# Performance work log

Measured on AMD Instinct MI355X. Metric: run time of the kernel, lower is better.

## Reference

```python
import jax, jax.numpy as jnp
import numpy as np

N_NODES = 200000
N_EDGES = 6400000
NUM_FEATURES = 128


def _glorot(key, fan_in, fan_out):
    return jax.random.normal(key, (fan_in, fan_out), jnp.float32) * (1.0 / np.sqrt(fan_in))


def gcn_conv(x, src, dst, W, b):
    """PyG GCNConv: h = D^{-1/2}(A+I)D^{-1/2} (x @ W) + b, self-loops added."""
    n = x.shape[0]
    ones = jnp.ones(src.shape, x.dtype)
    # degree after adding self-loops: 1 + in-degree (edges flow src -> dst)
    deg = 1.0 + jax.ops.segment_sum(ones, dst, num_segments=n)
    dinv = jax.lax.rsqrt(deg)  # deg >= 1, safe
    h = x @ W  # [n, out]
    norm = dinv[src] * dinv[dst]  # [E]
    msg = h[src] * norm[:, None]
    agg = jax.ops.segment_sum(msg, dst, num_segments=n)
    agg = agg + h * (dinv * dinv)[:, None]  # self-loop contribution
    return agg + b


def setup_inputs() -> dict:
    key = jax.random.key(0)
    ks = jax.random.split(key, 16)
    x = jax.random.normal(ks[0], (N_NODES, NUM_FEATURES), jnp.float32)
    edge_index = jax.random.randint(ks[1], (2, N_EDGES), 0, N_NODES, dtype=jnp.int64)
    params = {
        'W1': _glorot(ks[2], NUM_FEATURES, 64), 'b1': jnp.zeros((64,), jnp.float32),
        'W2': _glorot(ks[3], 64, 32),           'b2': jnp.zeros((32,), jnp.float32),
        'W3': _glorot(ks[4], 32, 16),           'b3': jnp.zeros((16,), jnp.float32),
        'Wsk02': _glorot(ks[5], NUM_FEATURES, 32), 'bsk02': jnp.zeros((32,), jnp.float32),
        'Wsk13': _glorot(ks[6], 64, 16),           'bsk13': jnp.zeros((16,), jnp.float32),
        'Wlin': _glorot(ks[7], 16, 1),             'blin': jnp.zeros((1,), jnp.float32),
    }
    return {'x': x, 'edge_index': edge_index, **params}


def reference(x, edge_index, W1, b1, W2, b2, W3, b3, Wsk02, bsk02, Wsk13, bsk13, Wlin, blin):
    # Dropout is identity in eval mode.
    src, dst = edge_index[0], edge_index[1]
    h1 = jax.nn.relu(gcn_conv(x, src, dst, W1, b1))
    h2 = jax.nn.relu(gcn_conv(h1, src, dst, W2, b2) + x @ Wsk02 + bsk02)
    h3 = jax.nn.relu(gcn_conv(h2, src, dst, W3, b3) + h1 @ Wsk13 + bsk13)
    return jax.nn.sigmoid(h3 @ Wlin + blin)  # [N, 1]
```

## Files before the change

kernel.cpp:

```cpp
#include <hip/hip_runtime.h>
#include <hip/hip_fp16.h>
#include <math.h>

#define MAXB 1024
#define MAXCB 128
#define TILE1 8192
#define SCAT_T 512
#define EPT1 (TILE1 / SCAT_T)
#define LCAP 13568
#define GCHUNK 4096

typedef _Float16 f16x8 __attribute__((ext_vector_type(8)));
typedef float f32x4 __attribute__((ext_vector_type(4)));


__device__ __forceinline__ unsigned int pack_f16(float a, float b) {
    __half2 h = __floats2half2_rn(a, b);
    return *reinterpret_cast<unsigned int*>(&h);
}
__device__ __forceinline__ float f16_lo(unsigned int u) {
    __half2 h = *reinterpret_cast<__half2*>(&u);
    return __low2float(h);
}
__device__ __forceinline__ float f16_hi(unsigned int u) {
    __half2 h = *reinterpret_cast<__half2*>(&u);
    return __high2float(h);
}
__device__ __forceinline__ void acc8(float* a, uint4 u) {
    a[0] += f16_lo(u.x); a[1] += f16_hi(u.x);
    a[2] += f16_lo(u.y); a[3] += f16_hi(u.y);
    a[4] += f16_lo(u.z); a[5] += f16_hi(u.z);
    a[6] += f16_lo(u.w); a[7] += f16_hi(u.w);
}
__device__ __forceinline__ void unpack8(uint4 u, float* v) {
    v[0] = f16_lo(u.x); v[1] = f16_hi(u.x);
    v[2] = f16_lo(u.y); v[3] = f16_hi(u.y);
    v[4] = f16_lo(u.z); v[5] = f16_hi(u.z);
    v[6] = f16_lo(u.w); v[7] = f16_hi(u.w);
}
__device__ __forceinline__ uint4 h2add4(uint4 a, uint4 b) {
    const __half2* pa = reinterpret_cast<const __half2*>(&a);
    const __half2* pb = reinterpret_cast<const __half2*>(&b);
    uint4 r;
    __half2* pr = reinterpret_cast<__half2*>(&r);
#pragma unroll
    for (int i = 0; i < 4; i++) pr[i] = __hadd2(pa[i], pb[i]);
    return r;
}
__device__ __forceinline__ unsigned int pkadd(unsigned int a, unsigned int b) {
    __half2 r = __hadd2(*reinterpret_cast<__half2*>(&a), *reinterpret_cast<__half2*>(&b));
    return *reinterpret_cast<unsigned int*>(&r);
}


__device__ __forceinline__ bool detect64(const int* __restrict__ ei) {
    int lane = threadIdx.x & 63;
    unsigned long long m = __ballot(ei[2 * lane + 1] != 0);
    return m == 0ull;
}

__device__ __forceinline__ int load_src(const int* ei, int e, bool is64, int i) {
    return is64 ? ei[2 * i] : ei[i];
}
__device__ __forceinline__ int load_dst(const int* ei, int e, bool is64, int i) {
    return is64 ? ei[2 * e + 2 * i] : ei[e + i];
}


__global__ __launch_bounds__(256) void bin_count(const int* __restrict__ ei, int e,
                                                 int shift, int* __restrict__ gcnt) {
    __shared__ int h[MAXB];
    for (int i = threadIdx.x; i < MAXB; i += 256) h[i] = 0;
    bool is64 = detect64(ei);
    __syncthreads();
    int stride = gridDim.x * 256;
    for (int i = blockIdx.x * 256 + threadIdx.x; i < e; i += stride) {
        int d = load_dst(ei, e, is64, i);
        atomicAdd(&h[d >> shift], 1);
    }
    __syncthreads();
    for (int i = threadIdx.x; i < MAXB; i += 256)
        if (h[i]) atomicAdd(&gcnt[i], h[i]);
}


__global__ void bin_scan_init(const int* __restrict__ gcnt, int nb, int ncb,
                              int* __restrict__ base, int* __restrict__ gcursor,
                              int* __restrict__ gcur1) {
    __shared__ int sh[1024];
    __shared__ int ex[1024];
    int t = threadIdx.x;
    int v = (t < nb) ? gcnt[t] : 0;
    sh[t] = v;
    __syncthreads();
    for (int off = 1; off < 1024; off <<= 1) {
        int x = (t >= off) ? sh[t - off] : 0;
        __syncthreads();
        sh[t] += x;
        __syncthreads();
    }
    int excl = sh[t] - v;
    ex[t] = excl;
    if (t < nb) {
        base[t] = excl;
        gcursor[t] = excl;
        if (t == nb - 1) base[nb] = sh[t];
    }
    __syncthreads();
    if (t < ncb) gcur1[t] = ex[8 * t];
}


__global__ __launch_bounds__(SCAT_T) void scatter_coarse(const int* __restrict__ ei, int e,
                                                         int shift,
                                                         int* __restrict__ gcur1,
                                                         unsigned int* __restrict__ gpk1) {
    __shared__ int hist[MAXCB];
    __shared__ int lbase[MAXCB];
    __shared__ int delta[MAXCB];
    __shared__ int cur[MAXCB];
    __shared__ unsigned int sbuf[TILE1];
    __shared__ unsigned char sbkt[TILE1];
    __shared__ int sh[SCAT_T];

    const int t = threadIdx.x;
    const int pkshift = shift + 3;
    const int pkmask = (1 << pkshift) - 1;
    const bool is64 = detect64(ei);
    const int tile0 = blockIdx.x * TILE1;
    const int cnt = min(TILE1, e - tile0);

    for (int i = t; i < MAXCB; i += SCAT_T) hist[i] = 0;
    __syncthreads();

    unsigned int pk[EPT1];
    int bk[EPT1];
#pragma unroll
    for (int k = 0; k < EPT1; k++) {
        int g = tile0 + k * SCAT_T + t;
        bk[k] = -1;
        if (g < e) {
            int s = load_src(ei, e, is64, g);
            int d = load_dst(ei, e, is64, g);
            pk[k] = ((unsigned int)s << pkshift) | (unsigned int)(d & pkmask);
            bk[k] = d >> pkshift;
            atomicAdd(&hist[bk[k]], 1);
        }
    }
    __syncthreads();

    {
        int v = (t < MAXCB) ? hist[t] : 0;
        sh[t] = v;
        __syncthreads();
        for (int off = 1; off < SCAT_T; off <<= 1) {
            int x = (t >= off) ? sh[t - off] : 0;
            __syncthreads();
            sh[t] += x;
            __syncthreads();
        }
        if (t < MAXCB) lbase[t] = sh[t] - v;
    }
    __syncthreads();

    if (t < MAXCB) {
        int c = hist[t];
        if (c > 0) delta[t] = atomicAdd(&gcur1[t], c) - lbase[t];
        cur[t] = lbase[t];
    }
    __syncthreads();

#pragma unroll
    for (int k = 0; k < EPT1; k++) {
        if (bk[k] >= 0) {
            int p = atomicAdd(&cur[bk[k]], 1);
            sbuf[p] = pk[k];
            sbkt[p] = (unsigned char)bk[k];
        }
    }
    __syncthreads();

    for (int i = t; i < cnt; i += SCAT_T)
        gpk1[delta[sbkt[i]] + i] = sbuf[i];
}


__global__ __launch_bounds__(SCAT_T) void scatter_fine(const unsigned int* __restrict__ gpk1,
                                                       const int* __restrict__ base,
                                                       int nbkt, int shift,
                                                       int* __restrict__ gcursor,
                                                       unsigned int* __restrict__ gpk2) {
    __shared__ int hist[8];
    __shared__ int lbase[8];
    __shared__ int delta[8];
    __shared__ int cur[8];
    __shared__ unsigned int sbuf[TILE1];
    __shared__ unsigned char sbkt[TILE1];

    const int t = threadIdx.x;
    const int cb = blockIdx.x >> 3;
    const int s = blockIdx.x & 7;
    const int f0 = 8 * cb;
    const int fhiIdx = min(f0 + 8, nbkt);
    const int lo = base[f0];
    const int hi = base[fhiIdx];
    const int len = hi - lo;
    const int slo = lo + (int)((long long)len * s / 8);
    const int shi = lo + (int)((long long)len * (s + 1) / 8);

    for (int tile0 = slo; tile0 < shi; tile0 += TILE1) {
        const int cnt = min(TILE1, shi - tile0);
        if (t < 8) hist[t] = 0;
        __syncthreads();

        unsigned int pk[EPT1];
        int bk[EPT1];
#pragma unroll
        for (int k = 0; k < EPT1; k++) {
            int li = k * SCAT_T + t;
            bk[k] = -1;
            if (li < cnt) {
                pk[k] = gpk1[tile0 + li];
                bk[k] = (pk[k] >> shift) & 7;
                atomicAdd(&hist[bk[k]], 1);
            }
        }
        __syncthreads();

        if (t == 0) {
            int run = 0;
            for (int f = 0; f < 8; f++) { lbase[f] = run; run += hist[f]; }
        }
        __syncthreads();
        if (t < 8) {
            int c = hist[t];
            if (c > 0) delta[t] = atomicAdd(&gcursor[f0 + t], c) - lbase[t];
            cur[t] = lbase[t];
        }
        __syncthreads();

#pragma unroll
        for (int k = 0; k < EPT1; k++) {
            if (bk[k] >= 0) {
                int p = atomicAdd(&cur[bk[k]], 1);
                sbuf[p] = pk[k];
                sbkt[p] = (unsigned char)bk[k];
            }
        }
        __syncthreads();

        for (int i = t; i < cnt; i += SCAT_T)
            gpk2[delta[sbkt[i]] + i] = sbuf[i];
        __syncthreads();
    }
}


__global__ __launch_bounds__(256) void bucket_build(const unsigned int* __restrict__ gpk,
                                                    const int* __restrict__ base, int shift,
                                                    int n, int e, float* __restrict__ dinv,
                                                    int* __restrict__ row_ptr,
                                                    int* __restrict__ col) {
    __shared__ int lcol[LCAP];
    __shared__ int dc[MAXB];
    __shared__ int cur[MAXB];
    __shared__ int sh[256];
    const int t = threadIdx.x;
    const int b = blockIdx.x;
    const int pkshift = shift + 3;
    const int mask = (1 << shift) - 1;
    const int width = 1 << shift;
    const int node0 = b << shift;
    const int nc = min(width, n - node0);
    const int lo = base[b], hi = base[b + 1];
    const int ecnt = hi - lo;

    for (int i = t; i < width; i += 256) dc[i] = 0;
    __syncthreads();
    for (int j = lo + t; j < hi; j += 256)
        atomicAdd(&dc[gpk[j] & mask], 1);
    __syncthreads();
    {
        int b4 = t * 4;
        int v0 = (b4 + 0 < width) ? dc[b4 + 0] : 0;
        int v1 = (b4 + 1 < width) ? dc[b4 + 1] : 0;
        int v2 = (b4 + 2 < width) ? dc[b4 + 2] : 0;
        int v3 = (b4 + 3 < width) ? dc[b4 + 3] : 0;
        int s = v0 + v1 + v2 + v3;
        sh[t] = s;
        __syncthreads();
        for (int off = 1; off < 256; off <<= 1) {
            int x = (t >= off) ? sh[t - off] : 0;
            __syncthreads();
            sh[t] += x;
            __syncthreads();
        }
        int excl = sh[t] - s;
        int pf[4] = {excl, excl + v0, excl + v0 + v1, excl + v0 + v1 + v2};
        int vv[4] = {v0, v1, v2, v3};
#pragma unroll
        for (int q = 0; q < 4; q++) {
            int i = b4 + q;
            if (i < nc) {
                row_ptr[node0 + i] = lo + pf[q];
                dinv[node0 + i] = rsqrtf(1.0f + (float)vv[q]);
            }
            if (i < width) cur[i] = pf[q];
        }
    }
    if (b == gridDim.x - 1 && t == 0) row_ptr[n] = e;
    __syncthreads();

    if (ecnt <= LCAP) {
        for (int j = lo + t; j < hi; j += 256) {
            unsigned int v = gpk[j];
            int p = atomicAdd(&cur[v & mask], 1);
            lcol[p] = (int)(v >> pkshift);
        }
        __syncthreads();
        for (int j = t; j < ecnt; j += 256)
            col[lo + j] = lcol[j];
    } else {
        for (int j = lo + t; j < hi; j += 256) {
            unsigned int v = gpk[j];
            int p = atomicAdd(&cur[v & mask], 1);
            col[lo + p] = (int)(v >> pkshift);
        }
    }
}


__global__ void prep_w(const float* __restrict__ W1, const float* __restrict__ Wsk02,
                       const float* __restrict__ W2, const float* __restrict__ Wsk13,
                       const float* __restrict__ W3, unsigned short* __restrict__ wt) {
    int i = blockIdx.x * 256 + threadIdx.x;
    float v;
    if (i < 12288) {
        int c = i >> 7, k = i & 127;
        v = (c < 64) ? W1[k * 64 + c] : Wsk02[k * 32 + (c - 64)];
    } else if (i < 15360) {
        int j = i - 12288;
        int c = j >> 6, k = j & 63;
        v = (c < 32) ? W2[k * 32 + c] : Wsk13[k * 16 + (c - 32)];
    } else if (i < 15872) {
        int j = i - 15360;
        int c = j >> 5, k = j & 31;
        v = W3[k * 16 + c];
    } else return;
    wt[i] = (unsigned short)pack_f16(v, 0.f);
}


template <int K, int CO1, int CO2, bool AHALF>
__global__ __launch_bounds__(256) void gemm_mfma(const void* __restrict__ Av,
                                                 const unsigned short* __restrict__ wt,
                                                 const float* __restrict__ dinv,
                                                 unsigned int* __restrict__ out1,
                                                 float* __restrict__ out2, int n) {
    constexpr int N = CO1 + CO2;
    constexpr int NCT = N / 16;
    constexpr int NK = K / 32;
    constexpr int CHK = K / 8;
    constexpr int SWZ = (CHK - 1) < 15 ? (CHK - 1) : 15;
    __shared__ __align__(16) unsigned char Ash[64 * K * 2];
    __shared__ __align__(16) unsigned char Bsh[N * K * 2];

    const int t = threadIdx.x;
    const int row0 = blockIdx.x * 64;

    for (int i = t; i < 64 * CHK; i += 256) {
        int r = i / CHK, c = i % CHK;
        int row = row0 + r;
        uint4 w{0u, 0u, 0u, 0u};
        if (row < n) {
            if (AHALF) {
                w = *reinterpret_cast<const uint4*>(
                    (const unsigned short*)Av + (size_t)row * K + c * 8);
            } else {
                const float* xr = (const float*)Av + (size_t)row * K + c * 8;
                float4 p = *reinterpret_cast<const float4*>(xr);
                float4 q = *reinterpret_cast<const float4*>(xr + 4);
                w.x = pack_f16(p.x, p.y); w.y = pack_f16(p.z, p.w);
                w.z = pack_f16(q.x, q.y); w.w = pack_f16(q.z, q.w);
            }
        }
        int addr = i * 16;
        addr ^= ((r & SWZ) << 4);
        *reinterpret_cast<uint4*>(&Ash[addr]) = w;
    }
    for (int i = t; i < N * CHK; i += 256) {
        int cc = i / CHK;
        uint4 w = *reinterpret_cast<const uint4*>(&wt[(i / CHK) * K + (i % CHK) * 8]);
        int addr = i * 16;
        addr ^= ((cc & SWZ) << 4);
        *reinterpret_cast<uint4*>(&Bsh[addr]) = w;
    }
    __syncthreads();

    const int wv = t >> 6;
    const int lane = t & 63;
    const int lrow = wv * 16 + (lane & 15);
    const int kb = (lane >> 4) * 16;

    f16x8 afr[NK];
#pragma unroll
    for (int s = 0; s < NK; s++) {
        int addr = lrow * (2 * K) + s * 64 + kb;
        addr ^= ((lrow & SWZ) << 4);
        afr[s] = *reinterpret_cast<const f16x8*>(&Ash[addr]);
    }

    f32x4 acc[NCT];
#pragma unroll
    for (int ct = 0; ct < NCT; ct++) acc[ct] = f32x4{0.f, 0.f, 0.f, 0.f};

#pragma unroll
    for (int ct = 0; ct < NCT; ct++) {
        int cc = ct * 16 + (lane & 15);
#pragma unroll
        for (int s = 0; s < NK; s++) {
            int addr = cc * (2 * K) + s * 64 + kb;
            addr ^= ((cc & SWZ) << 4);
            f16x8 bfr = *reinterpret_cast<const f16x8*>(&Bsh[addr]);
            acc[ct] = __builtin_amdgcn_mfma_f32_16x16x32_f16(afr[s], bfr, acc[ct], 0, 0, 0);
        }
    }

    const int rbase = row0 + wv * 16 + (lane >> 4) * 4;
    const int cidx = lane & 15;
    float dn[4];
#pragma unroll
    for (int r = 0; r < 4; r++) dn[r] = (rbase + r < n) ? dinv[rbase + r] : 0.f;

#pragma unroll
    for (int ct = 0; ct < NCT; ct++) {
        int col = ct * 16 + cidx;
        if (col < CO1) {
#pragma unroll
            for (int r = 0; r < 4; r++) {
                float v = acc[ct][r] * dn[r];
                float o = __shfl_xor(v, 1);
                int row = rbase + r;
                if (!(lane & 1) && row < n)
                    out1[(size_t)row * (CO1 / 2) + ct * 8 + cidx / 2] = pack_f16(v, o);
            }
        } else if (CO2 > 0) {
#pragma unroll
            for (int r = 0; r < 4; r++) {
                int row = rbase + r;
                if (row < n) out2[(size_t)row * CO2 + (col - CO1)] = acc[ct][r];
            }
        }
    }
}


template <int F, bool FINAL, bool PACKOUT>
__global__ __launch_bounds__(256) void gather_combine(
    const uint4* __restrict__ hp4, const int* __restrict__ row_ptr,
    const int* __restrict__ col, const float* __restrict__ dinv,
    const float* __restrict__ bias, const float* __restrict__ sk,
    const float* __restrict__ bsk, void* __restrict__ outv,
    const float* __restrict__ Wlin, const float* __restrict__ blin, int n) {
    constexpr int L = F / 8;
    constexpr int EPW = 64 / L;
    int wid = (blockIdx.x * blockDim.x + threadIdx.x) >> 6;
    int lane = threadIdx.x & 63;
    if (wid >= n) return;
    int s = lane / L;
    int el = lane % L;
    int start = row_ptr[wid];
    int end = row_ptr[wid + 1];

    float a[8] = {0.f, 0.f, 0.f, 0.f, 0.f, 0.f, 0.f, 0.f};
    const uint4 z4{0u, 0u, 0u, 0u};
    for (int j = start + s; j < end; j += 4 * EPW) {
        int j1 = j + EPW, j2 = j + 2 * EPW, j3 = j + 3 * EPW;
        bool v1 = j1 < end, v2 = j2 < end, v3 = j3 < end;
        int c0 = col[j];
        int c1 = col[v1 ? j1 : j];
        int c2 = col[v2 ? j2 : j];
        int c3 = col[v3 ? j3 : j];
        uint4 u0 = hp4[(size_t)c0 * L + el];
        uint4 u1 = hp4[(size_t)c1 * L + el];
        uint4 u2 = hp4[(size_t)c2 * L + el];
        uint4 u3 = hp4[(size_t)c3 * L + el];
        if (!v1) u1 = z4;
        if (!v2) u2 = z4;
        if (!v3) u3 = z4;
        uint4 t01 = h2add4(u0, u1);
        uint4 t23 = h2add4(u2, u3);
        acc8(a, h2add4(t01, t23));
    }

#pragma unroll
    for (int m = L; m < 64; m <<= 1) {
#pragma unroll
        for (int q = 0; q < 8; q++) a[q] += __shfl_xor(a[q], m);
    }

    if (lane < L) {
        float dn = dinv[wid];
        uint4 us = hp4[(size_t)wid * L + el];
        float v[8];
        unpack8(us, v);
        float4 b0 = *reinterpret_cast<const float4*>(&bias[8 * el]);
        float4 b1 = *reinterpret_cast<const float4*>(&bias[8 * el + 4]);
        float o[8];
        o[0] = dn * a[0] + v[0] * dn + b0.x;
        o[1] = dn * a[1] + v[1] * dn + b0.y;
        o[2] = dn * a[2] + v[2] * dn + b0.z;
        o[3] = dn * a[3] + v[3] * dn + b0.w;
        o[4] = dn * a[4] + v[4] * dn + b1.x;
        o[5] = dn * a[5] + v[5] * dn + b1.y;
        o[6] = dn * a[6] + v[6] * dn + b1.z;
        o[7] = dn * a[7] + v[7] * dn + b1.w;
        if (sk) {
            float4 s0 = *reinterpret_cast<const float4*>(&sk[(size_t)wid * F + 8 * el]);
            float4 s1 = *reinterpret_cast<const float4*>(&sk[(size_t)wid * F + 8 * el + 4]);
            float4 k0 = *reinterpret_cast<const float4*>(&bsk[8 * el]);
            float4 k1 = *reinterpret_cast<const float4*>(&bsk[8 * el + 4]);
            o[0] += s0.x + k0.x; o[1] += s0.y + k0.y;
            o[2] += s0.z + k0.z; o[3] += s0.w + k0.w;
            o[4] += s1.x + k1.x; o[5] += s1.y + k1.y;
            o[6] += s1.z + k1.z; o[7] += s1.w + k1.w;
        }
#pragma unroll
        for (int q = 0; q < 8; q++) o[q] = fmaxf(o[q], 0.f);
        if (FINAL) {
            float4 wl0 = *reinterpret_cast<const float4*>(&Wlin[8 * el]);
            float4 wl1 = *reinterpret_cast<const float4*>(&Wlin[8 * el + 4]);
            float d = o[0] * wl0.x + o[1] * wl0.y + o[2] * wl0.z + o[3] * wl0.w +
                      o[4] * wl1.x + o[5] * wl1.y + o[6] * wl1.z + o[7] * wl1.w;
            d += __shfl_xor(d, 1);
            if (el == 0) ((float*)outv)[wid] = 1.0f / (1.0f + expf(-(d + blin[0])));
        } else if (PACKOUT) {
            uint4 pk{pack_f16(o[0], o[1]), pack_f16(o[2], o[3]),
                     pack_f16(o[4], o[5]), pack_f16(o[6], o[7])};
            ((uint4*)outv)[(size_t)wid * L + el] = pk;
        } else {
            float* out = (float*)outv;
            float4 w0{o[0], o[1], o[2], o[3]};
            float4 w1{o[4], o[5], o[6], o[7]};
            *reinterpret_cast<float4*>(&out[(size_t)wid * F + 8 * el]) = w0;
            *reinterpret_cast<float4*>(&out[(size_t)wid * F + 8 * el + 4]) = w1;
        }
    }
}


template <int F, int T, bool FINAL, bool PACKOUT>
__global__ __launch_bounds__(256) void gather_tpn(
    const uint4* __restrict__ hp4, const int* __restrict__ row_ptr,
    const int* __restrict__ col, const float* __restrict__ dinv,
    const float* __restrict__ bias, const float* __restrict__ sk,
    const float* __restrict__ bsk, void* __restrict__ outv,
    const float* __restrict__ Wlin, const float* __restrict__ blin, int n) {
    constexpr int L = F / 8;
    constexpr int NPB = 256 / T;
    __shared__ int lcol[GCHUNK];
    const int t = threadIdx.x;
    const int sub = t & (T - 1);
    const int node0 = blockIdx.x * NPB;
    const int node = node0 + (t / T);
    const int hiN = min(node0 + NPB, n);
    const int lo = row_ptr[node0];
    const int hi = row_ptr[hiN];

    int start = 0, end = 0;
    if (node < n) { start = row_ptr[node]; end = row_ptr[node + 1]; }

    unsigned int acc[F / 2];
#pragma unroll
    for (int q = 0; q < F / 2; q++) acc[q] = 0u;

    for (int ch = lo; ch < hi; ch += GCHUNK) {
        int cnt = min(GCHUNK, hi - ch);
        __syncthreads();
        for (int i = t; i < cnt; i += 256) lcol[i] = col[ch + i];
        __syncthreads();
        int first = start + sub;
        if (first < ch) first += ((ch - first + T - 1) & ~(T - 1));
        int last = min(end, ch + cnt);
        int j = first;
        if (j < last) {
            uint4 u[L];
            {
                const uint4* rp = hp4 + (size_t)lcol[j - ch] * L;
#pragma unroll
                for (int w = 0; w < L; w++) u[w] = rp[w];
            }
            for (j += T; j < last; j += T) {
                uint4 v[L];
                const uint4* rq = hp4 + (size_t)lcol[j - ch] * L;
#pragma unroll
                for (int w = 0; w < L; w++) v[w] = rq[w];
#pragma unroll
                for (int w = 0; w < L; w++) {
                    acc[4 * w + 0] = pkadd(acc[4 * w + 0], u[w].x);
                    acc[4 * w + 1] = pkadd(acc[4 * w + 1], u[w].y);
                    acc[4 * w + 2] = pkadd(acc[4 * w + 2], u[w].z);
                    acc[4 * w + 3] = pkadd(acc[4 * w + 3], u[w].w);
                }
#pragma unroll
                for (int w = 0; w < L; w++) u[w] = v[w];
            }
#pragma unroll
            for (int w = 0; w < L; w++) {
                acc[4 * w + 0] = pkadd(acc[4 * w + 0], u[w].x);
                acc[4 * w + 1] = pkadd(acc[4 * w + 1], u[w].y);
                acc[4 * w + 2] = pkadd(acc[4 * w + 2], u[w].z);
                acc[4 * w + 3] = pkadd(acc[4 * w + 3], u[w].w);
            }
        }
    }

#pragma unroll
    for (int m = 1; m < T; m <<= 1) {
#pragma unroll
        for (int q = 0; q < F / 2; q++) {
            unsigned int o = (unsigned int)__shfl_xor((int)acc[q], m);
            acc[q] = pkadd(acc[q], o);
        }
    }

    if (node < n && sub == 0) {
        float dn = dinv[node];
        const uint4* sp = hp4 + (size_t)node * L;
        float o[F];
#pragma unroll
        for (int w = 0; w < L; w++) {
            uint4 u = sp[w];
            float sv[8];
            unpack8(u, sv);
#pragma unroll
            for (int q = 0; q < 8; q++) {
                int f = w * 8 + q;
                float av = (q & 1) ? f16_hi(acc[4 * w + (q >> 1)])
                                   : f16_lo(acc[4 * w + (q >> 1)]);
                o[f] = dn * (av + sv[q]) + bias[f];
            }
        }
        if (sk) {
#pragma unroll
            for (int f = 0; f < F; f++)
                o[f] += sk[(size_t)node * F + f] + bsk[f];
        }
#pragma unroll
        for (int f = 0; f < F; f++) o[f] = fmaxf(o[f], 0.f);

        if (FINAL) {
            float d = blin[0];
#pragma unroll
            for (int f = 0; f < F; f++) d += o[f] * Wlin[f];
            ((float*)outv)[node] = 1.0f / (1.0f + expf(-d));
        } else if (PACKOUT) {
            uint4* o4 = (uint4*)outv + (size_t)node * L;
#pragma unroll
            for (int w = 0; w < L; w++) {
                uint4 pk{pack_f16(o[w * 8 + 0], o[w * 8 + 1]),
                         pack_f16(o[w * 8 + 2], o[w * 8 + 3]),
                         pack_f16(o[w * 8 + 4], o[w * 8 + 5]),
                         pack_f16(o[w * 8 + 6], o[w * 8 + 7])};
                o4[w] = pk;
            }
        }
    }
}


extern "C" void kernel_launch(void* const* d_in, const int* in_sizes, int n_in,
                              void* d_out, int out_size, void* d_ws, size_t ws_size,
                              hipStream_t stream) {
    const float* x     = (const float*)d_in[0];
    const int*   ei    = (const int*)d_in[1];
    const float* W1    = (const float*)d_in[2];
    const float* b1    = (const float*)d_in[3];
    const float* W2    = (const float*)d_in[4];
    const float* b2    = (const float*)d_in[5];
    const float* W3    = (const float*)d_in[6];
    const float* b3    = (const float*)d_in[7];
    const float* Wsk02 = (const float*)d_in[8];
    const float* bsk02 = (const float*)d_in[9];
    const float* Wsk13 = (const float*)d_in[10];
    const float* bsk13 = (const float*)d_in[11];
    const float* Wlin  = (const float*)d_in[12];
    const float* blin  = (const float*)d_in[13];

    const int n = in_sizes[0] / 128;
    const int e = in_sizes[1] / 2;

    int shift = 8;
    while (((n + (1 << shift) - 1) >> shift) > MAXB) shift++;
    const int nbkt = (n + (1 << shift) - 1) >> shift;
    const int ncb = (nbkt + 7) / 8;

    char* p = (char*)d_ws;
    auto alloc = [&](size_t bytes) {
        void* r = (void*)p;
        p += (bytes + 255) / 256 * 256;
        return r;
    };
    int*   gcnt    = (int*)alloc(MAXB * 4);
    int*   base    = (int*)alloc((MAXB + 1) * 4);
    int*   gcursor = (int*)alloc(MAXB * 4);
    int*   gcur1   = (int*)alloc(MAXCB * 4);
    unsigned short* wt = (unsigned short*)alloc(15872 * 2);
    int*   row_ptr = (int*)alloc((size_t)(n + 1) * 4);
    float* dinv    = (float*)alloc((size_t)n * 4);
    int*   col     = (int*)alloc((size_t)e * 4);
    size_t h1b     = (size_t)e * 4 > (size_t)n * 128 ? (size_t)e * 4 : (size_t)n * 128;
    unsigned int* h1 = (unsigned int*)alloc(h1b);
    unsigned int* h2 = (unsigned int*)alloc((size_t)n * 64);
    float* sk02    = (float*)alloc((size_t)n * 32 * 4);
    float* sk13    = (float*)alloc((size_t)n * 16 * 4);
    size_t prebytes = (size_t)e * 4 > (size_t)n * 128 ? (size_t)e * 4 : (size_t)n * 128;
    unsigned int* preb = (unsigned int*)alloc(prebytes);
    unsigned int* gpk1 = h1;
    unsigned int* gpk2 = preb;

    auto cdiv = [](int a, int b) { return (a + b - 1) / b; };

    prep_w<<<62, 256, 0, stream>>>(W1, Wsk02, W2, Wsk13, W3, wt);

    hipMemsetAsync(gcnt, 0, MAXB * 4, stream);
    bin_count<<<1024, 256, 0, stream>>>(ei, e, shift, gcnt);
    bin_scan_init<<<1, 1024, 0, stream>>>(gcnt, nbkt, ncb, base, gcursor, gcur1);
    scatter_coarse<<<cdiv(e, TILE1), SCAT_T, 0, stream>>>(ei, e, shift, gcur1, gpk1);
    scatter_fine<<<ncb * 8, SCAT_T, 0, stream>>>(gpk1, base, nbkt, shift, gcursor, gpk2);
    bucket_build<<<nbkt, 256, 0, stream>>>(gpk2, base, shift, n, e, dinv, row_ptr, col);

    gemm_mfma<128, 64, 32, false><<<cdiv(n, 64), 256, 0, stream>>>(
        x, wt, dinv, preb, sk02, n);
    gather_combine<64, false, true><<<cdiv(n, 4), 256, 0, stream>>>(
        (const uint4*)preb, row_ptr, col, dinv, b1, nullptr, nullptr, h1, nullptr, nullptr, n);

    gemm_mfma<64, 32, 16, true><<<cdiv(n, 64), 256, 0, stream>>>(
        h1, wt + 12288, dinv, preb, sk13, n);
    gather_tpn<32, 4, false, true><<<cdiv(n, 64), 256, 0, stream>>>(
        (const uint4*)preb, row_ptr, col, dinv, b2, sk02, bsk02, h2, nullptr, nullptr, n);

    gemm_mfma<32, 16, 0, true><<<cdiv(n, 64), 256, 0, stream>>>(
        h2, wt + 15360, dinv, preb, sk13, n);
    gather_tpn<16, 4, true, false><<<cdiv(n, 64), 256, 0, stream>>>(
        (const uint4*)preb, row_ptr, col, dinv, b3, sk13, bsk13, d_out, Wlin, blin, n);
}
```

Measured before the change: 456.8 us.

## Store skip-connection outputs in fp16 and widen threads-per-node in gather kernels

The GEMM kernels now pack the skip-branch outputs (sk02, sk13) as fp16 pairs instead of fp32, which halves their write traffic and the read traffic in the later gather kernels. gather_tpn reads these packed halves and unpacks them. The gather_tpn launches also go from 4 to 8 threads per node, with twice as many blocks, which changes how the per-node edge loop is spread across threads. Unused skip and final-output paths are removed from gather_combine. The cost is lower precision in the skip terms and possibly more per-node reduction overhead.

```diff
diff --git a/kernel.cpp b/kernel.cpp
--- a/kernel.cpp
+++ b/kernel.cpp
@@ -356,7 +356,7 @@
                                                  const unsigned short* __restrict__ wt,
                                                  const float* __restrict__ dinv,
                                                  unsigned int* __restrict__ out1,
-                                                 float* __restrict__ out2, int n) {
+                                                 unsigned int* __restrict__ out2, int n) {
     constexpr int N = CO1 + CO2;
     constexpr int NCT = N / 16;
     constexpr int NK = K / 32;
@@ -447,21 +447,23 @@
         } else if (CO2 > 0) {
 #pragma unroll
             for (int r = 0; r < 4; r++) {
+                float v = acc[ct][r];
+                float o = __shfl_xor(v, 1);
                 int row = rbase + r;
-                if (row < n) out2[(size_t)row * CO2 + (col - CO1)] = acc[ct][r];
-            }
-        }
-    }
-}
-
-
-template <int F, bool FINAL, bool PACKOUT>
+                if (!(lane & 1) && row < n)
+                    out2[(size_t)row * (CO2 / 2) + (ct * 16 + cidx - CO1) / 2] =
+                        pack_f16(v, o);
+            }
+        }
+    }
+}
+
+
+template <int F, bool PACKOUT>
 __global__ __launch_bounds__(256) void gather_combine(
     const uint4* __restrict__ hp4, const int* __restrict__ row_ptr,
     const int* __restrict__ col, const float* __restrict__ dinv,
-    const float* __restrict__ bias, const float* __restrict__ sk,
-    const float* __restrict__ bsk, void* __restrict__ outv,
-    const float* __restrict__ Wlin, const float* __restrict__ blin, int n) {
+    const float* __restrict__ bias, void* __restrict__ outv, int n) {
     constexpr int L = F / 8;
     constexpr int EPW = 64 / L;
     int wid = (blockIdx.x * blockDim.x + threadIdx.x) >> 6;
@@ -515,26 +517,9 @@
         o[5] = dn * a[5] + v[5] * dn + b1.y;
         o[6] = dn * a[6] + v[6] * dn + b1.z;
         o[7] = dn * a[7] + v[7] * dn + b1.w;
-        if (sk) {
-            float4 s0 = *reinterpret_cast<const float4*>(&sk[(size_t)wid * F + 8 * el]);
-            float4 s1 = *reinterpret_cast<const float4*>(&sk[(size_t)wid * F + 8 * el + 4]);
-            float4 k0 = *reinterpret_cast<const float4*>(&bsk[8 * el]);
-            float4 k1 = *reinterpret_cast<const float4*>(&bsk[8 * el + 4]);
-            o[0] += s0.x + k0.x; o[1] += s0.y + k0.y;
-            o[2] += s0.z + k0.z; o[3] += s0.w + k0.w;
-            o[4] += s1.x + k1.x; o[5] += s1.y + k1.y;
-            o[6] += s1.z + k1.z; o[7] += s1.w + k1.w;
-        }
 #pragma unroll
         for (int q = 0; q < 8; q++) o[q] = fmaxf(o[q], 0.f);
-        if (FINAL) {
-            float4 wl0 = *reinterpret_cast<const float4*>(&Wlin[8 * el]);
-            float4 wl1 = *reinterpret_cast<const float4*>(&Wlin[8 * el + 4]);
-            float d = o[0] * wl0.x + o[1] * wl0.y + o[2] * wl0.z + o[3] * wl0.w +
-                      o[4] * wl1.x + o[5] * wl1.y + o[6] * wl1.z + o[7] * wl1.w;
-            d += __shfl_xor(d, 1);
-            if (el == 0) ((float*)outv)[wid] = 1.0f / (1.0f + expf(-(d + blin[0])));
-        } else if (PACKOUT) {
+        if (PACKOUT) {
             uint4 pk{pack_f16(o[0], o[1]), pack_f16(o[2], o[3]),
                      pack_f16(o[4], o[5]), pack_f16(o[6], o[7])};
             ((uint4*)outv)[(size_t)wid * L + el] = pk;
@@ -553,7 +538,7 @@
 __global__ __launch_bounds__(256) void gather_tpn(
     const uint4* __restrict__ hp4, const int* __restrict__ row_ptr,
     const int* __restrict__ col, const float* __restrict__ dinv,
-    const float* __restrict__ bias, const float* __restrict__ sk,
+    const float* __restrict__ bias, const uint4* __restrict__ skh,
     const float* __restrict__ bsk, void* __restrict__ outv,
     const float* __restrict__ Wlin, const float* __restrict__ blin, int n) {
     constexpr int L = F / 8;
@@ -641,10 +626,16 @@
                 o[f] = dn * (av + sv[q]) + bias[f];
             }
         }
-        if (sk) {
-#pragma unroll
-            for (int f = 0; f < F; f++)
-                o[f] += sk[(size_t)node * F + f] + bsk[f];
+        if (skh) {
+            const uint4* skp = skh + (size_t)node * L;
+#pragma unroll
+            for (int w = 0; w < L; w++) {
+                float sv2[8];
+                unpack8(skp[w], sv2);
+#pragma unroll
+                for (int q = 0; q < 8; q++)
+                    o[w * 8 + q] += sv2[q] + bsk[w * 8 + q];
+            }
         }
 #pragma unroll
         for (int f = 0; f < F; f++) o[f] = fmaxf(o[f], 0.f);
@@ -712,8 +703,8 @@
     size_t h1b     = (size_t)e * 4 > (size_t)n * 128 ? (size_t)e * 4 : (size_t)n * 128;
     unsigned int* h1 = (unsigned int*)alloc(h1b);
     unsigned int* h2 = (unsigned int*)alloc((size_t)n * 64);
-    float* sk02    = (float*)alloc((size_t)n * 32 * 4);
-    float* sk13    = (float*)alloc((size_t)n * 16 * 4);
+    unsigned int* sk02 = (unsigned int*)alloc((size_t)n * 64);
+    unsigned int* sk13 = (unsigned int*)alloc((size_t)n * 32);
     size_t prebytes = (size_t)e * 4 > (size_t)n * 128 ? (size_t)e * 4 : (size_t)n * 128;
     unsigned int* preb = (unsigned int*)alloc(prebytes);
     unsigned int* gpk1 = h1;
@@ -732,16 +723,18 @@
 
     gemm_mfma<128, 64, 32, false><<<cdiv(n, 64), 256, 0, stream>>>(
         x, wt, dinv, preb, sk02, n);
-    gather_combine<64, false, true><<<cdiv(n, 4), 256, 0, stream>>>(
-        (const uint4*)preb, row_ptr, col, dinv, b1, nullptr, nullptr, h1, nullptr, nullptr, n);
+    gather_combine<64, true><<<cdiv(n, 4), 256, 0, stream>>>(
+        (const uint4*)preb, row_ptr, col, dinv, b1, h1, n);
 
     gemm_mfma<64, 32, 16, true><<<cdiv(n, 64), 256, 0, stream>>>(
         h1, wt + 12288, dinv, preb, sk13, n);
-    gather_tpn<32, 4, false, true><<<cdiv(n, 64), 256, 0, stream>>>(
-        (const uint4*)preb, row_ptr, col, dinv, b2, sk02, bsk02, h2, nullptr, nullptr, n);
+    gather_tpn<32, 8, false, true><<<cdiv(n, 32), 256, 0, stream>>>(
+        (const uint4*)preb, row_ptr, col, dinv, b2, (const uint4*)sk02, bsk02,
+        h2, nullptr, nullptr, n);
 
     gemm_mfma<32, 16, 0, true><<<cdiv(n, 64), 256, 0, stream>>>(
         h2, wt + 15360, dinv, preb, sk13, n);
-    gather_tpn<16, 4, true, false><<<cdiv(n, 64), 256, 0, stream>>>(
-        (const uint4*)preb, row_ptr, col, dinv, b3, sk13, bsk13, d_out, Wlin, blin, n);
-}
+    gather_tpn<16, 8, true, false><<<cdiv(n, 32), 256, 0, stream>>>(
+        (const uint4*)preb, row_ptr, col, dinv, b3, (const uint4*)sk13, bsk13,
+        d_out, Wlin, blin, n);
+}
```

Measured after the change: 448.7 us (median of 2 runs). About the same (-1.8%).
